# Optimization experiments

Measured on AMD Instinct MI355X. Metric: run time of the kernel, lower is better.

Reference implementation:

```python
import jax, jax.numpy as jnp
import numpy as np

IMAGE_SIZE = 256
NEAR = 0.1
FAR = 100.0
EPS = 1e-3
BACKGROUND = (0.0, 0.0, 0.0)
CHUNK = 64   # faces per scan step (bounds peak memory of the z-buffer pass)
TINY = 1e-12


def _bary(vx, vy, vz, xp, yp):
    """Barycentric weights / perspective-correct depth at pixel centers.
    vx, vy, vz: 3-tuples of vertex coords, broadcastable with xp/yp.
    Mirrors the CUDA kernel: unnormalized cross-product weights, normalize,
    clamp to [0,1], renormalize, zp = 1 / sum(w_k / z_k), near/far clip."""
    x0, x1, x2 = vx; y0, y1, y2 = vy; z0, z1, z2 = vz
    w0 = yp * (x2 - x1) + xp * (y1 - y2) + (x1 * y2 - x2 * y1)
    w1 = yp * (x0 - x2) + xp * (y2 - y0) + (x2 * y0 - x0 * y2)
    w2 = yp * (x1 - x0) + xp * (y0 - y1) + (x0 * y1 - x1 * y0)
    det = w0 + w1 + w2
    safe_det = jnp.where(jnp.abs(det) > TINY, det, 1.0)
    n0, n1, n2 = w0 / safe_det, w1 / safe_det, w2 / safe_det
    inside = (n0 > 0) & (n1 > 0) & (n2 > 0) & (jnp.abs(det) > TINY)
    n0 = jnp.clip(n0, 0.0, 1.0); n1 = jnp.clip(n1, 0.0, 1.0); n2 = jnp.clip(n2, 0.0, 1.0)
    s = n0 + n1 + n2
    s = jnp.where(s > TINY, s, 1.0)
    n0, n1, n2 = n0 / s, n1 / s, n2 / s
    inv_zp = n0 / z0 + n1 / z1 + n2 / z2
    inv_zp = jnp.where(jnp.abs(inv_zp) > TINY, inv_zp, 1.0)
    zp = 1.0 / inv_zp
    valid = inside & (zp > NEAR) & (zp < FAR)
    return (n0, n1, n2), zp, valid


def _pixel_coords():
    IS = IMAGE_SIZE
    return (2.0 * jnp.arange(IS, dtype=jnp.float32) + 1.0 - IS) / IS


def _forward(faces, textures):
    B, F = faces.shape[:2]
    IS = IMAGE_SIZE
    ii = _pixel_coords()

    # ---- pass 1: z-buffer (face-index argmin), chunked scan over faces ----
    # index selection is non-differentiable -> stop_gradient keeps vjp cheap
    fsg = jax.lax.stop_gradient(faces)
    n_chunks = F // CHUNK
    fchunks = jnp.transpose(fsg.reshape(B, n_chunks, CHUNK, 3, 3), (1, 0, 2, 3, 4))
    bases = jnp.arange(n_chunks, dtype=jnp.int32) * CHUNK
    xp4 = ii[None, None, None, :]
    yp4 = ii[None, None, :, None]

    def step(carry, inp):
        depth, fidx = carry
        fc, base = inp                               # fc: [B, CHUNK, 3, 3]
        vx = tuple(fc[:, :, k, 0][:, :, None, None] for k in range(3))
        vy = tuple(fc[:, :, k, 1][:, :, None, None] for k in range(3))
        vz = tuple(fc[:, :, k, 2][:, :, None, None] for k in range(3))
        _, zp, valid = _bary(vx, vy, vz, xp4, yp4)   # [B, CHUNK, IS, IS]
        zp = jnp.where(valid, zp, jnp.inf)
        local = jnp.argmin(zp, axis=1).astype(jnp.int32)
        zbest = jnp.min(zp, axis=1)
        better = zbest < depth
        depth = jnp.where(better, zbest, depth)
        fidx = jnp.where(better, base + local, fidx)
        return (depth, fidx), None

    init = (jnp.full((B, IS, IS), FAR, jnp.float32),
            jnp.full((B, IS, IS), -1, jnp.int32))
    (_, fidx), _ = jax.lax.scan(step, init, (fchunks, bases))

    # ---- pass 2: differentiable recompute for winning faces ----
    mask = fidx >= 0
    safe_idx = jnp.maximum(fidx, 0)
    fsel = jnp.take_along_axis(
        faces.reshape(B, F, 9), safe_idx.reshape(B, -1, 1), axis=1
    ).reshape(B, IS, IS, 3, 3)
    vx = tuple(fsel[..., k, 0] for k in range(3))
    vy = tuple(fsel[..., k, 1] for k in range(3))
    vz = tuple(fsel[..., k, 2] for k in range(3))
    w, zp, _ = _bary(vx, vy, vz, ii[None, None, :], ii[None, :, None])
    depth_map = jnp.where(mask, zp, FAR)

    # ---- texture sampling: 8-corner trilinear in the T^3 face texel cube ----
    T = textures.shape[2]
    tif = [jnp.clip(w[k] * (T - 1) * zp / vz[k], 0.0, T - 1 - EPS) for k in range(3)]
    lo = [jnp.floor(t) for t in tif]
    fr = [t - l for t, l in zip(tif, lo)]
    lo = [l.astype(jnp.int32) for l in lo]

    tex_flat = textures.reshape(B, F * T * T * T, 3)
    base_idx = safe_idx * (T * T * T)
    rgb = jnp.zeros((B, IS, IS, 3), faces.dtype)
    for d0 in (0, 1):
        for d1 in (0, 1):
            for d2 in (0, 1):
                wgt = ((fr[0] if d0 else 1.0 - fr[0]) *
                       (fr[1] if d1 else 1.0 - fr[1]) *
                       (fr[2] if d2 else 1.0 - fr[2]))
                idx = base_idx + (lo[0] + d0) * T * T + (lo[1] + d1) * T + (lo[2] + d2)
                smp = jnp.take_along_axis(tex_flat, idx.reshape(B, -1, 1), axis=1)
                rgb = rgb + wgt[..., None] * smp.reshape(B, IS, IS, 3)

    bg = jnp.asarray(BACKGROUND, faces.dtype)
    mf = mask.astype(faces.dtype)[..., None]
    rgb_map = rgb * mf + (1.0 - mf) * bg
    alpha_map = mask.astype(faces.dtype)
    # pack (rgb, alpha, depth) into a single [B, IS, IS, 5] tensor
    return jnp.concatenate([rgb_map, alpha_map[..., None], depth_map[..., None]], axis=-1)


def setup_inputs() -> dict:
    key = jax.random.key(0)
    B, F, T = 4, 4096, 4
    k1, k2, k3, k4, k5 = jax.random.split(key, 5)
    # small triangles scattered over the screen with depths in (near, far)
    ctr = jax.random.uniform(k1, (B, F, 1, 2), minval=-0.95, maxval=0.95)
    off = jax.random.uniform(k2, (B, F, 3, 2), minval=-0.08, maxval=0.08)
    xy = ctr + off
    zc = jax.random.uniform(k3, (B, F, 1, 1), minval=1.0, maxval=50.0)
    zo = jax.random.uniform(k4, (B, F, 3, 1), minval=-0.2, maxval=0.2)
    faces = jnp.concatenate([xy, zc + zo], axis=-1).astype(jnp.float32)
    textures = jax.random.uniform(k5, (B, F, T, T, T, 3), dtype=jnp.float32)
    return {"faces": faces, "textures": textures}


def reference(faces, textures):
    return _forward(faces, textures)
```

## Files before the change

### kernel.cpp

```cpp
#include <hip/hip_runtime.h>

#define IS 256
#define FCOUNT 4096
#define NEARP 0.1f
#define FARP 100.0f
#define TINYF 1e-12f
#define CAP 256
#define GCAP 128
#define DET_GLOBAL 1e-5f

__device__ __forceinline__ float frn(float r) { asm("" : "+v"(r)); return r; }
__device__ __forceinline__ float mulrn(float a, float b) { return frn(a * b); }
__device__ __forceinline__ float addrn(float a, float b) { return frn(a + b); }
__device__ __forceinline__ float subrn(float a, float b) { return frn(a - b); }
__device__ __forceinline__ float divrn(float a, float b) { return frn(a / b); }
__device__ __forceinline__ float fmarn(float a, float b, float c) {
    return frn(__builtin_fmaf(a, b, c));
}

__global__ __launch_bounds__(64) void bin_kernel(
    const float* __restrict__ faces,
    float4* __restrict__ cA, float4* __restrict__ cB, float4* __restrict__ cC,
    int* __restrict__ counts, int* __restrict__ lists,
    int* __restrict__ gcount, int* __restrict__ glist, int B, int F)
{
    const int gid = blockIdx.x * 64 + threadIdx.x;
    if (gid >= B * F) return;
    const int b = gid >> 12, f = gid & (FCOUNT - 1);
    const float* fp = faces + (size_t)gid * 9;
    const float x0 = fp[0], y0 = fp[1], z0 = fp[2];
    const float x1 = fp[3], y1 = fp[4], z1 = fp[5];
    const float x2 = fp[6], y2 = fp[7], z2 = fp[8];

    const float A0 = subrn(x2, x1), B0 = subrn(y1, y2);
    const float C0 = fmarn(x1, y2, -mulrn(x2, y1));
    const float A1 = subrn(x0, x2), B1 = subrn(y2, y0);
    const float C1 = fmarn(x2, y0, -mulrn(x0, y2));
    const float A2 = subrn(x1, x0), B2 = subrn(y0, y1);
    const float C2 = fmarn(x0, y1, -mulrn(x1, y0));
    cA[gid] = make_float4(A0, B0, C0, A1);
    cB[gid] = make_float4(B1, C1, A2, B2);
    cC[gid] = make_float4(C2, z0, z1, z2);

    const float det = (x1 - x0) * (y2 - y0) - (x2 - x0) * (y1 - y0);
    const float ad = fabsf(det);
    if (ad < DET_GLOBAL) {
        const int pos = atomicAdd(&gcount[b], 1);
        if (pos < GCAP) glist[b * GCAP + pos] = f;
        return;
    }
    const float d = 2e-3f + 3e-7f / ad;
    const float lox = fminf(x0, fminf(x1, x2)) - d;
    const float hix = fmaxf(x0, fmaxf(x1, x2)) + d;
    const float loy = fminf(y0, fminf(y1, y2)) - d;
    const float hiy = fmaxf(y0, fmaxf(y1, y2)) + d;
    int tx0 = (int)floorf((256.f * lox + 255.f) * (1.f / 32.f));
    int tx1 = (int)floorf((256.f * hix + 255.f) * (1.f / 32.f));
    int ty0 = (int)floorf((256.f * loy + 255.f) * (1.f / 32.f));
    int ty1 = (int)floorf((256.f * hiy + 255.f) * (1.f / 32.f));
    tx0 = max(tx0, 0); tx1 = min(tx1, 15);
    ty0 = max(ty0, 0); ty1 = min(ty1, 15);
    for (int ty = ty0; ty <= ty1; ++ty)
        for (int tx = tx0; tx <= tx1; ++tx) {
            const int t = (b * 16 + ty) * 16 + tx;
            const int pos = atomicAdd(&counts[t], 1);
            if (pos < CAP) lists[(size_t)t * CAP + pos] = f;
        }
}

__global__ __launch_bounds__(256) void raster_kernel(
    const float* __restrict__ faces,
    const float* __restrict__ textures,
    const float4* __restrict__ cA, const float4* __restrict__ cB,
    const float4* __restrict__ cC,
    const int* __restrict__ counts, const int* __restrict__ lists,
    const int* __restrict__ gcount, const int* __restrict__ glist,
    float* __restrict__ out, int B, int F)
{
    const int tid  = threadIdx.x;
    const int b    = blockIdx.x >> 8;
    const int tile = blockIdx.x & 255;
    const int px   = (tile & 15) * 16 + (tid & 15);
    const int py   = (tile >> 4) * 16 + (tid >> 4);
    const float xp = (float)(2 * px + 1 - IS) * (1.0f / IS);
    const float yp = (float)(2 * py + 1 - IS) * (1.0f / IS);

    __shared__ float4 s_a[256];
    __shared__ float4 s_b[256];
    __shared__ float4 s_c[256];
    __shared__ int    s_idx[256];

    float bestz = FARP;
    int   besti = -1;

    const int cnt  = min(counts[blockIdx.x], CAP);
    const int gcnt = min(gcount[b], GCAP);
    const int total = cnt + gcnt;
    const int* mylist = lists + (size_t)blockIdx.x * CAP;
    const int* gl     = glist + b * GCAP;
    const int fb = b * F;

    for (int cbase = 0; cbase < total; cbase += 256) {
        const int m = min(total - cbase, 256);
        if (tid < m) {
            const int k = cbase + tid;
            const int f = (k < cnt) ? mylist[k] : gl[k - cnt];
            s_a[tid] = cA[fb + f];
            s_b[tid] = cB[fb + f];
            s_c[tid] = cC[fb + f];
            s_idx[tid] = f;
        }
        __syncthreads();

        for (int j = 0; j < m; ++j) {
            const float4 fa = s_a[j];
            const float4 fb4 = s_b[j];
            const float4 fc = s_c[j];
            const float w0 = addrn(fmarn(yp, fa.x, mulrn(xp, fa.y)), fa.z);
            const float w1 = addrn(fmarn(yp, fa.w, mulrn(xp, fb4.x)), fb4.y);
            const float w2 = addrn(fmarn(yp, fb4.z, mulrn(xp, fb4.w)), fc.x);
            const float det = addrn(addrn(w0, w1), w2);
            bool ins;
            if (det > TINYF)       ins = (w0 > 0.f) && (w1 > 0.f) && (w2 > 0.f);
            else if (det < -TINYF) ins = (w0 < 0.f) && (w1 < 0.f) && (w2 < 0.f);
            else                   ins = false;
            if (ins) {
                float n0 = divrn(w0, det), n1 = divrn(w1, det), n2 = divrn(w2, det);
                n0 = frn(fminf(fmaxf(n0, 0.f), 1.f));
                n1 = frn(fminf(fmaxf(n1, 0.f), 1.f));
                n2 = frn(fminf(fmaxf(n2, 0.f), 1.f));
                float s = addrn(addrn(n0, n1), n2);
                s = (s > TINYF) ? s : 1.0f;
                n0 = divrn(n0, s); n1 = divrn(n1, s); n2 = divrn(n2, s);
                float iz = addrn(addrn(divrn(n0, fc.y), divrn(n1, fc.z)),
                                 divrn(n2, fc.w));
                iz = (fabsf(iz) > TINYF) ? iz : 1.0f;
                const float zp = divrn(1.0f, iz);
                if (zp > NEARP && zp < FARP) {
                    const int fi = s_idx[j];
                    if (zp < bestz || (zp == bestz && fi < besti)) {
                        bestz = zp;
                        besti = fi;
                    }
                }
            }
        }
        __syncthreads();
    }

    const float* fbase = faces + (size_t)b * F * 9;
    float r = 0.f, g = 0.f, bch = 0.f, alpha = 0.f, depth = FARP;
    if (besti >= 0) {
        const float* fp = fbase + (size_t)besti * 9;
        const float x0 = fp[0], y0 = fp[1], z0 = fp[2];
        const float x1 = fp[3], y1 = fp[4], z1 = fp[5];
        const float x2 = fp[6], y2 = fp[7], z2 = fp[8];
        const float w0 = addrn(fmarn(yp, subrn(x2, x1), mulrn(xp, subrn(y1, y2))),
                               fmarn(x1, y2, -mulrn(x2, y1)));
        const float w1 = addrn(fmarn(yp, subrn(x0, x2), mulrn(xp, subrn(y2, y0))),
                               fmarn(x2, y0, -mulrn(x0, y2)));
        const float w2 = addrn(fmarn(yp, subrn(x1, x0), mulrn(xp, subrn(y0, y1))),
                               fmarn(x0, y1, -mulrn(x1, y0)));
        const float det = addrn(addrn(w0, w1), w2);
        const float sd = (fabsf(det) > TINYF) ? det : 1.0f;
        float n0 = divrn(w0, sd), n1 = divrn(w1, sd), n2 = divrn(w2, sd);
        n0 = frn(fminf(fmaxf(n0, 0.f), 1.f));
        n1 = frn(fminf(fmaxf(n1, 0.f), 1.f));
        n2 = frn(fminf(fmaxf(n2, 0.f), 1.f));
        float s = addrn(addrn(n0, n1), n2);
        s = (s > TINYF) ? s : 1.0f;
        n0 = divrn(n0, s); n1 = divrn(n1, s); n2 = divrn(n2, s);
        float iz = addrn(addrn(divrn(n0, z0), divrn(n1, z1)), divrn(n2, z2));
        iz = (fabsf(iz) > TINYF) ? iz : 1.0f;
        const float zp = divrn(1.0f, iz);
        depth = zp;

        const float t0 = fminf(fmaxf(divrn(mulrn(mulrn(n0, 3.0f), zp), z0), 0.f), 2.999f);
        const float t1 = fminf(fmaxf(divrn(mulrn(mulrn(n1, 3.0f), zp), z1), 0.f), 2.999f);
        const float t2 = fminf(fmaxf(divrn(mulrn(mulrn(n2, 3.0f), zp), z2), 0.f), 2.999f);
        const float l0 = floorf(t0), l1 = floorf(t1), l2 = floorf(t2);
        const float fr0 = subrn(t0, l0), fr1 = subrn(t1, l1), fr2 = subrn(t2, l2);
        const int i0 = (int)l0, i1 = (int)l1, i2 = (int)l2;

        const float* tx = textures + (size_t)(b * F + besti) * 64 * 3;
        for (int d0 = 0; d0 < 2; ++d0)
            for (int d1 = 0; d1 < 2; ++d1)
                for (int d2 = 0; d2 < 2; ++d2) {
                    const float wg = mulrn(mulrn(d0 ? fr0 : subrn(1.0f, fr0),
                                                 d1 ? fr1 : subrn(1.0f, fr1)),
                                           d2 ? fr2 : subrn(1.0f, fr2));
                    const float* tp = tx + ((i0 + d0) * 16 + (i1 + d1) * 4 + (i2 + d2)) * 3;
                    r   = addrn(r,   mulrn(wg, tp[0]));
                    g   = addrn(g,   mulrn(wg, tp[1]));
                    bch = addrn(bch, mulrn(wg, tp[2]));
                }
        alpha = 1.0f;
    }

    float* op = out + (((size_t)b * IS + py) * IS + px) * 5;
    op[0] = r;
    op[1] = g;
    op[2] = bch;
    op[3] = alpha;
    op[4] = depth;
}

extern "C" void kernel_launch(void* const* d_in, const int* in_sizes, int n_in,
                              void* d_out, int out_size, void* d_ws, size_t ws_size,
                              hipStream_t stream) {
    const float* faces    = (const float*)d_in[0];
    const float* textures = (const float*)d_in[1];
    float* out = (float*)d_out;
    const int F = FCOUNT;
    const int B = in_sizes[0] / (F * 9);
    const int ntiles = B * 256;

    int* counts = (int*)d_ws;
    int* gcount = counts + ntiles;
    int* glist  = gcount + B;
    int* lists  = glist + B * GCAP;
    float4* cA  = (float4*)(lists + (size_t)ntiles * CAP);
    float4* cB  = cA + (size_t)B * F;
    float4* cC  = cB + (size_t)B * F;

    hipMemsetAsync(counts, 0, (size_t)(ntiles + B) * sizeof(int), stream);
    bin_kernel<<<dim3((B * F + 63) / 64), dim3(64), 0, stream>>>(
        faces, cA, cB, cC, counts, lists, gcount, glist, B, F);
    raster_kernel<<<dim3(ntiles), dim3(256), 0, stream>>>(
        faces, textures, cA, cB, cC, counts, lists, gcount, glist, out, B, F);
}
```

Measured before the change: 109.1 us.

## Bin faces into 8x8 tiles processed per wave with depth early-out

Binning moves from 16x16-pixel tiles to 8x8-pixel tiles (32x32 bins per image) with tighter ceil/floor pixel-center bounds. Each wavefront of a 256-thread block now handles its own 8x8 bin, with per-wave shared staging and wave barriers in place of block-wide __syncthreads. A conservative depth early-out skips the barycentric divides when a face's minimum vertex z exceeds the current best. The aim is to test fewer faces per pixel and remove block synchronisation, at the cost of more atomics in binning and a smaller per-bin CAP that could overflow.

```diff
diff --git a/kernel.cpp b/kernel.cpp
--- a/kernel.cpp
+++ b/kernel.cpp
@@ -5,9 +5,10 @@
 #define NEARP 0.1f
 #define FARP 100.0f
 #define TINYF 1e-12f
-#define CAP 256
+#define CAP 192
 #define GCAP 128
 #define DET_GLOBAL 1e-5f
+#define ZEPS 2e-4f
 
 __device__ __forceinline__ float frn(float r) { asm("" : "+v"(r)); return r; }
 __device__ __forceinline__ float mulrn(float a, float b) { return frn(a * b); }
@@ -54,15 +55,15 @@
     const float hix = fmaxf(x0, fmaxf(x1, x2)) + d;
     const float loy = fminf(y0, fminf(y1, y2)) - d;
     const float hiy = fmaxf(y0, fmaxf(y1, y2)) + d;
-    int tx0 = (int)floorf((256.f * lox + 255.f) * (1.f / 32.f));
-    int tx1 = (int)floorf((256.f * hix + 255.f) * (1.f / 32.f));
-    int ty0 = (int)floorf((256.f * loy + 255.f) * (1.f / 32.f));
-    int ty1 = (int)floorf((256.f * hiy + 255.f) * (1.f / 32.f));
-    tx0 = max(tx0, 0); tx1 = min(tx1, 15);
-    ty0 = max(ty0, 0); ty1 = min(ty1, 15);
+    int tx0 = (int)ceilf ((256.f * lox + 241.f) * (1.f / 16.f));
+    int tx1 = (int)floorf((256.f * hix + 255.f) * (1.f / 16.f));
+    int ty0 = (int)ceilf ((256.f * loy + 241.f) * (1.f / 16.f));
+    int ty1 = (int)floorf((256.f * hiy + 255.f) * (1.f / 16.f));
+    tx0 = max(tx0, 0); tx1 = min(tx1, 31);
+    ty0 = max(ty0, 0); ty1 = min(ty1, 31);
     for (int ty = ty0; ty <= ty1; ++ty)
         for (int tx = tx0; tx <= tx1; ++tx) {
-            const int t = (b * 16 + ty) * 16 + tx;
+            const int t = (b * 32 + ty) * 32 + tx;
             const int pos = atomicAdd(&counts[t], 1);
             if (pos < CAP) lists[(size_t)t * CAP + pos] = f;
         }
@@ -78,44 +79,49 @@
     float* __restrict__ out, int B, int F)
 {
     const int tid  = threadIdx.x;
+    const int lane = tid & 63;
+    const int w    = tid >> 6;
     const int b    = blockIdx.x >> 8;
     const int tile = blockIdx.x & 255;
-    const int px   = (tile & 15) * 16 + (tid & 15);
-    const int py   = (tile >> 4) * 16 + (tid >> 4);
+    const int qtx  = 2 * (tile & 15) + (w & 1);
+    const int qty  = 2 * (tile >> 4) + (w >> 1);
+    const int qbin = (b * 32 + qty) * 32 + qtx;
+    const int px   = qtx * 8 + (lane & 7);
+    const int py   = qty * 8 + (lane >> 3);
     const float xp = (float)(2 * px + 1 - IS) * (1.0f / IS);
     const float yp = (float)(2 * py + 1 - IS) * (1.0f / IS);
 
-    __shared__ float4 s_a[256];
-    __shared__ float4 s_b[256];
-    __shared__ float4 s_c[256];
-    __shared__ int    s_idx[256];
+    __shared__ float4 s_a[4][64];
+    __shared__ float4 s_b[4][64];
+    __shared__ float4 s_c[4][64];
+    __shared__ int    s_i[4][64];
 
     float bestz = FARP;
     int   besti = -1;
 
-    const int cnt  = min(counts[blockIdx.x], CAP);
+    const int cnt  = min(counts[qbin], CAP);
     const int gcnt = min(gcount[b], GCAP);
     const int total = cnt + gcnt;
-    const int* mylist = lists + (size_t)blockIdx.x * CAP;
+    const int* mylist = lists + (size_t)qbin * CAP;
     const int* gl     = glist + b * GCAP;
     const int fb = b * F;
 
-    for (int cbase = 0; cbase < total; cbase += 256) {
-        const int m = min(total - cbase, 256);
-        if (tid < m) {
-            const int k = cbase + tid;
+    for (int cb = 0; cb < total; cb += 64) {
+        const int m = min(total - cb, 64);
+        if (lane < m) {
+            const int k = cb + lane;
             const int f = (k < cnt) ? mylist[k] : gl[k - cnt];
-            s_a[tid] = cA[fb + f];
-            s_b[tid] = cB[fb + f];
-            s_c[tid] = cC[fb + f];
-            s_idx[tid] = f;
+            s_a[w][lane] = cA[fb + f];
+            s_b[w][lane] = cB[fb + f];
+            s_c[w][lane] = cC[fb + f];
+            s_i[w][lane] = f;
         }
-        __syncthreads();
+        __builtin_amdgcn_wave_barrier();
 
         for (int j = 0; j < m; ++j) {
-            const float4 fa = s_a[j];
-            const float4 fb4 = s_b[j];
-            const float4 fc = s_c[j];
+            const float4 fa  = s_a[w][j];
+            const float4 fb4 = s_b[w][j];
+            const float4 fc  = s_c[w][j];
             const float w0 = addrn(fmarn(yp, fa.x, mulrn(xp, fa.y)), fa.z);
             const float w1 = addrn(fmarn(yp, fa.w, mulrn(xp, fb4.x)), fb4.y);
             const float w2 = addrn(fmarn(yp, fb4.z, mulrn(xp, fb4.w)), fc.x);
@@ -124,7 +130,8 @@
             if (det > TINYF)       ins = (w0 > 0.f) && (w1 > 0.f) && (w2 > 0.f);
             else if (det < -TINYF) ins = (w0 < 0.f) && (w1 < 0.f) && (w2 < 0.f);
             else                   ins = false;
-            if (ins) {
+            const float minz = fminf(fminf(fc.y, fc.z), fc.w);
+            if (ins && minz <= bestz + ZEPS) {
                 float n0 = divrn(w0, det), n1 = divrn(w1, det), n2 = divrn(w2, det);
                 n0 = frn(fminf(fmaxf(n0, 0.f), 1.f));
                 n1 = frn(fminf(fmaxf(n1, 0.f), 1.f));
@@ -137,7 +144,7 @@
                 iz = (fabsf(iz) > TINYF) ? iz : 1.0f;
                 const float zp = divrn(1.0f, iz);
                 if (zp > NEARP && zp < FARP) {
-                    const int fi = s_idx[j];
+                    const int fi = s_i[w][j];
                     if (zp < bestz || (zp == bestz && fi < besti)) {
                         bestz = zp;
                         besti = fi;
@@ -145,7 +152,7 @@
                 }
             }
         }
-        __syncthreads();
+        __builtin_amdgcn_wave_barrier();
     }
 
     const float* fbase = faces + (size_t)b * F * 9;
@@ -213,19 +220,19 @@
     float* out = (float*)d_out;
     const int F = FCOUNT;
     const int B = in_sizes[0] / (F * 9);
-    const int ntiles = B * 256;
+    const int nbins = B * 1024;
 
     int* counts = (int*)d_ws;
-    int* gcount = counts + ntiles;
+    int* gcount = counts + nbins;
     int* glist  = gcount + B;
     int* lists  = glist + B * GCAP;
-    float4* cA  = (float4*)(lists + (size_t)ntiles * CAP);
+    float4* cA  = (float4*)(lists + (size_t)nbins * CAP);
     float4* cB  = cA + (size_t)B * F;
     float4* cC  = cB + (size_t)B * F;
 
-    hipMemsetAsync(counts, 0, (size_t)(ntiles + B) * sizeof(int), stream);
+    hipMemsetAsync(counts, 0, (size_t)(nbins + B) * sizeof(int), stream);
     bin_kernel<<<dim3((B * F + 63) / 64), dim3(64), 0, stream>>>(
         faces, cA, cB, cC, counts, lists, gcount, glist, B, F);
-    raster_kernel<<<dim3(ntiles), dim3(256), 0, stream>>>(
+    raster_kernel<<<dim3(B * 256), dim3(256), 0, stream>>>(
         faces, textures, cA, cB, cC, counts, lists, gcount, glist, out, B, F);
 }
```

New measurement: 99.57 us. 8.7% less time.
